# Kernel tuning notes

Hardware: AMD Instinct MI355X
Metric: run time of the kernel (lower is better)

Reference implementation:

```python
import jax, jax.numpy as jnp
import numpy as np

D_MODEL = 1024
NUM_HEADS = 16
D_K = D_MODEL // NUM_HEADS
THETA = 10000.0
BATCH = 2
SEQ = 2048


def apply_rope(x, token_positions):
    # x: [B, H, S, D_K]; token_positions: [S] int
    half = D_K // 2
    inv_freq = THETA ** (-(jnp.arange(half, dtype=jnp.float32) * 2.0) / D_K)  # [half]
    angles = token_positions.astype(jnp.float32)[:, None] * inv_freq[None, :]  # [S, half]
    cos = jnp.cos(angles)  # [S, half]
    sin = jnp.sin(angles)
    x1 = x[..., 0::2]  # even indices
    x2 = x[..., 1::2]  # odd indices
    out_even = x1 * cos - x2 * sin
    out_odd = x1 * sin + x2 * cos
    # interleave back: [..., S, half, 2] -> [..., S, D_K]
    return jnp.stack([out_even, out_odd], axis=-1).reshape(x.shape)


def setup_inputs() -> dict:
    key = jax.random.key(0)
    ks = jax.random.split(key, 5)
    x = jax.random.normal(ks[0], (BATCH, SEQ, D_MODEL), dtype=jnp.float32)
    token_positions = jnp.arange(SEQ, dtype=jnp.int64)
    scale = 0.02
    Wq = jax.random.normal(ks[1], (D_MODEL, D_MODEL), dtype=jnp.float32) * scale
    Wk = jax.random.normal(ks[2], (D_MODEL, D_MODEL), dtype=jnp.float32) * scale
    Wv = jax.random.normal(ks[3], (D_MODEL, D_MODEL), dtype=jnp.float32) * scale
    Wo = jax.random.normal(ks[4], (D_MODEL, D_MODEL), dtype=jnp.float32) * scale
    return {"x": x, "token_positions": token_positions, "Wq": Wq, "Wk": Wk, "Wv": Wv, "Wo": Wo}


def reference(x, token_positions, Wq, Wk, Wv, Wo):
    B, S, _ = x.shape
    # cs336 Linear: y = x @ W.T with W of shape (out, in), no bias
    def proj(W):
        h = jnp.einsum('bsd,od->bso', x, W)
        return h.reshape(B, S, NUM_HEADS, D_K).transpose(0, 2, 1, 3)  # [B,H,S,Dk]
    Q = apply_rope(proj(Wq), token_positions)
    K = apply_rope(proj(Wk), token_positions)
    V = proj(Wv)
    scores = jnp.einsum('bhqd,bhkd->bhqk', Q, K) / jnp.sqrt(jnp.float32(D_K))
    causal = jnp.tril(jnp.ones((S, S), dtype=bool))
    scores = jnp.where(causal, scores, -jnp.inf)
    attn = jax.nn.softmax(scores, axis=-1)
    out = jnp.einsum('bhqk,bhkd->bhqd', attn, V)  # [B,H,S,Dk]
    out = out.transpose(0, 2, 1, 3).reshape(B, S, D_MODEL)
    return jnp.einsum('bsd,od->bso', out, Wo)
```

## Files before the change

kernel.cpp:

```cpp
#include <hip/hip_runtime.h>
#include <hip/hip_bf16.h>
#include <math.h>

#define NHEADS 16
#define DKH 64
#define SEQ 2048
#define DMODEL 1024

typedef __attribute__((ext_vector_type(8))) short short8;
typedef __attribute__((ext_vector_type(4))) float f32x4;

#define GLDS16(g, l)                                         \
  __builtin_amdgcn_global_load_lds(                          \
      (__attribute__((address_space(1))) void*)(void*)(g),   \
      (__attribute__((address_space(3))) void*)(l), 16, 0, 0)

__device__ __forceinline__ short f2bf(float f) {
  unsigned u = __float_as_uint(f);
  unsigned r = (u + 0x7fffu + ((u >> 16) & 1u)) >> 16;
  return (short)r;
}

__device__ __forceinline__ short8 pack8(float4 a, float4 b) {
  short8 v;
  v[0] = f2bf(a.x); v[1] = f2bf(a.y); v[2] = f2bf(a.z); v[3] = f2bf(a.w);
  v[4] = f2bf(b.x); v[5] = f2bf(b.y); v[6] = f2bf(b.z); v[7] = f2bf(b.w);
  return v;
}

__device__ __forceinline__ int swz(int r, int gran) {
  return r * 64 + ((gran ^ (r & 7)) << 3);
}

__global__ __launch_bounds__(256) void precast_rope_kernel(
    const float* __restrict__ X, const float* __restrict__ Wq,
    const float* __restrict__ Wk, const float* __restrict__ Wv,
    const float* __restrict__ Wo, const int* __restrict__ tp,
    short* __restrict__ Xb, short* __restrict__ Wqb, short* __restrict__ Wkb,
    short* __restrict__ Wvb, short* __restrict__ Wob,
    float* __restrict__ ct, float* __restrict__ st) {
  int bid = blockIdx.x;
  if (bid < 4096) {
    int i = bid * 256 + threadIdx.x;
    const float* src; short* dst; int off;
    if (i < 524288) { src = X; dst = Xb; off = i; }
    else {
      int k = i - 524288; int w = k >> 17; off = k & 131071;
      src = (w == 0) ? Wq : (w == 1) ? Wk : (w == 2) ? Wv : Wo;
      dst = (w == 0) ? Wqb : (w == 1) ? Wkb : (w == 2) ? Wvb : Wob;
    }
    const float4* p = reinterpret_cast<const float4*>(src) + 2 * (size_t)off;
    float4 a = p[0], b = p[1];
    reinterpret_cast<short8*>(dst)[off] = pack8(a, b);
  } else {
    int idx = (bid - 4096) * 256 + threadIdx.x;
    if (idx >= SEQ * 32) return;
    int s = idx >> 5, i = idx & 31;
    int is64 = (tp[1] == 0);
    int p = is64 ? tp[2 * s] : tp[s];
    float invf = powf(10000.0f, -(2.0f * (float)i) / 64.0f);
    float a = (float)p * invf;
    ct[idx] = cosf(a);
    st[idx] = sinf(a);
  }
}

__global__ __launch_bounds__(512, 2) void gemm_qkv_kernel(
    const short* __restrict__ X, const short* __restrict__ Wq,
    const short* __restrict__ Wk, const short* __restrict__ Wv,
    short* __restrict__ Qb, short* __restrict__ Kb, short* __restrict__ Vb,
    const float* __restrict__ ct, const float* __restrict__ st) {
  __shared__ __align__(16) short As[2][256 * 64];
  __shared__ __align__(16) short Bs[2][256 * 64];
  const int tm = blockIdx.x;
  const int tn = blockIdx.y;
  const int tid = threadIdx.x;
  const int wave = tid >> 6, lane = tid & 63;
  const int l15 = lane & 15, quad = lane >> 4;
  const int wm = wave >> 2, wn = wave & 3;

  const int mid = tn >> 2;
  const int n0 = (tn & 3) * 256;
  const short* W = (mid == 0) ? Wq : (mid == 1 ? Wk : Wv);
  const short* Abase = X + (size_t)(tm * 256) * DMODEL;
  const short* Bbase = W + (size_t)n0 * DMODEL;

  const int lr = lane >> 3;
  const int lc = (lane & 7) ^ lr;

#define STG(SRC, DST, bufi, half, kt_)                                     \
  do {                                                                     \
    int R0 = (half) * 128 + wave * 16;                                     \
    GLDS16((SRC) + (size_t)(R0 + lr) * DMODEL + (kt_) * 64 + lc * 8,       \
           &DST[bufi][R0 * 64 + lane * 8]);                                \
    GLDS16((SRC) + (size_t)(R0 + 8 + lr) * DMODEL + (kt_) * 64 + lc * 8,   \
           &DST[bufi][(R0 + 8) * 64 + lane * 8]);                          \
  } while (0)

  f32x4 acc[8][4];
#pragma unroll
  for (int m = 0; m < 8; m++)
#pragma unroll
    for (int n = 0; n < 4; n++) acc[m][n] = (f32x4){0.f, 0.f, 0.f, 0.f};

  STG(Bbase, Bs, 0, 0, 0); STG(Bbase, Bs, 0, 1, 0);
  STG(Abase, As, 0, 0, 0); STG(Abase, As, 0, 1, 0);
  STG(Bbase, Bs, 1, 0, 1); STG(Bbase, Bs, 1, 1, 1);

  short8 bfr[4][2];
  for (int kt = 0; kt < 16; kt++) {
    const int buf = kt & 1;
    if (kt < 15) { STG(Abase, As, buf ^ 1, 0, kt + 1); }
    if (kt < 15) { asm volatile("s_waitcnt vmcnt(6)" ::: "memory"); }
    else         { asm volatile("s_waitcnt vmcnt(0)" ::: "memory"); }
    asm volatile("s_barrier" ::: "memory");
#pragma unroll
    for (int nb = 0; nb < 4; nb++)
#pragma unroll
      for (int ks = 0; ks < 2; ks++)
        bfr[nb][ks] = *reinterpret_cast<const short8*>(
            &Bs[buf][swz(wn * 64 + nb * 16 + l15, ks * 4 + quad)]);
    {
      short8 af[2][2];
#pragma unroll
      for (int j = 0; j < 2; j++)
#pragma unroll
        for (int ks = 0; ks < 2; ks++)
          af[j][ks] = *reinterpret_cast<const short8*>(
              &As[buf][swz(wm * 128 + j * 16 + l15, ks * 4 + quad)]);
      __builtin_amdgcn_s_setprio(1);
#pragma unroll
      for (int j = 0; j < 2; j++)
#pragma unroll
        for (int nb = 0; nb < 4; nb++)
#pragma unroll
          for (int ks = 0; ks < 2; ks++)
            acc[j][nb] = __builtin_amdgcn_mfma_f32_16x16x32_bf16(
                af[j][ks], bfr[nb][ks], acc[j][nb], 0, 0, 0);
      __builtin_amdgcn_s_setprio(0);
    }
    asm volatile("s_barrier" ::: "memory");
#pragma unroll
    for (int p = 1; p < 4; p++) {
      short8 af[2][2];
#pragma unroll
      for (int j = 0; j < 2; j++)
#pragma unroll
        for (int ks = 0; ks < 2; ks++)
          af[j][ks] = *reinterpret_cast<const short8*>(
              &As[buf][swz(wm * 128 + (p * 2 + j) * 16 + l15, ks * 4 + quad)]);
      if (p == 1)      { if (kt < 15) { STG(Abase, As, buf ^ 1, 1, kt + 1); } }
      else if (p == 2) { if (kt < 14) { STG(Bbase, Bs, buf, 0, kt + 2); } }
      else             { if (kt < 14) { STG(Bbase, Bs, buf, 1, kt + 2); } }
      asm volatile("s_barrier" ::: "memory");
      __builtin_amdgcn_s_setprio(1);
#pragma unroll
      for (int j = 0; j < 2; j++)
#pragma unroll
        for (int nb = 0; nb < 4; nb++)
#pragma unroll
          for (int ks = 0; ks < 2; ks++)
            acc[p * 2 + j][nb] = __builtin_amdgcn_mfma_f32_16x16x32_bf16(
                af[j][ks], bfr[nb][ks], acc[p * 2 + j][nb], 0, 0, 0);
      __builtin_amdgcn_s_setprio(0);
      asm volatile("s_barrier" ::: "memory");
    }
  }
#undef STG

#pragma unroll
  for (int mf = 0; mf < 8; mf++) {
    const int s0g = tm * 256 + wm * 128 + mf * 16 + quad * 4;
    const int b = s0g >> 11, s = s0g & 2047;
#pragma unroll
    for (int nb = 0; nb < 4; nb++) {
      int nl = n0 + wn * 64 + nb * 16 + l15;
      int h = nl >> 6, dd = nl & 63;
      if (mid == 2) {
        unsigned u0 = (unsigned)(unsigned short)f2bf(acc[mf][nb][0]) |
                      ((unsigned)(unsigned short)f2bf(acc[mf][nb][1]) << 16);
        unsigned u1 = (unsigned)(unsigned short)f2bf(acc[mf][nb][2]) |
                      ((unsigned)(unsigned short)f2bf(acc[mf][nb][3]) << 16);
        uint2 pk; pk.x = u0; pk.y = u1;
        *reinterpret_cast<uint2*>(Vb + ((size_t)(b * NHEADS + h) * DKH + dd) * SEQ + s) = pk;
      } else {
#pragma unroll
        for (int reg = 0; reg < 4; reg++) {
          float v = acc[mf][nb][reg];
          float pv = __shfl_xor(v, 1);
          int fi = dd >> 1;
          int sg = s + reg;
          float c = ct[sg * 32 + fi], sn = st[sg * 32 + fi];
          float o = (dd & 1) ? (pv * sn + v * c) : (v * c - pv * sn);
          size_t oi = (((size_t)(b * NHEADS + h)) * SEQ + sg) * DKH + dd;
          ((mid == 0) ? Qb : Kb)[oi] = f2bf(o);
        }
      }
    }
  }
}

__global__ __launch_bounds__(256, 4) void attn_kernel(
    const short* __restrict__ Qb, const short* __restrict__ Kb,
    const short* __restrict__ Vtb, short* __restrict__ Ob) {
  __shared__ __align__(16) short QPs[64 * 64];
  __shared__ __align__(16) short Ks[2][64 * 64];
  __shared__ __align__(16) short Vs[2][64 * 64];

  const int id = blockIdx.x;
  const int xx = id & 7;
  const int mm = (((id >> 3) & 3) + (id >> 8)) & 3;
  const int bh = id >> 5;
  const int qt = (mm == 0) ? (31 - xx) : (mm == 1) ? (16 + xx)
               : (mm == 2) ? (15 - xx) : xx;

  const int tid = threadIdx.x;
  const int wave = tid >> 6, lane = tid & 63;
  const int l15 = lane & 15, quad = lane >> 4;
  const int sr0 = tid >> 3, sc = tid & 7;

  const short* Qp = Qb + (size_t)bh * SEQ * DKH;
  const short* Kp = Kb + (size_t)bh * SEQ * DKH;
  const short* Vp = Vtb + (size_t)bh * DKH * SEQ;

  uint4 kreg[2], vreg[2];
#pragma unroll
  for (int i = 0; i < 2; i++) {
    int r = sr0 + i * 32;
    kreg[i] = *reinterpret_cast<const uint4*>(Kp + (size_t)r * DKH + sc * 8);
    vreg[i] = *reinterpret_cast<const uint4*>(Vp + (size_t)r * SEQ + sc * 8);
  }
#pragma unroll
  for (int i = 0; i < 2; i++) {
    int r = sr0 + i * 32;
    uint4 v = *reinterpret_cast<const uint4*>(Qp + (size_t)(qt * 64 + r) * DKH + sc * 8);
    *reinterpret_cast<uint4*>(&QPs[swz(r, sc)]) = v;
  }
#pragma unroll
  for (int i = 0; i < 2; i++) {
    int r = sr0 + i * 32;
    *reinterpret_cast<uint4*>(&Ks[0][swz(r, sc)]) = kreg[i];
    *reinterpret_cast<uint4*>(&Vs[0][swz(r, sc)]) = vreg[i];
  }
  __syncthreads();
  short8 qf0, qf1;
  {
    int r = wave * 16 + l15;
    qf0 = *reinterpret_cast<const short8*>(&QPs[swz(r, quad)]);
    qf1 = *reinterpret_cast<const short8*>(&QPs[swz(r, 4 + quad)]);
  }

  f32x4 accO[4];
#pragma unroll
  for (int i = 0; i < 4; i++) accO[i] = (f32x4){0.f, 0.f, 0.f, 0.f};
  float rs = 0.f;

  const float SCL = 0.125f * 1.44269504089f;
  const float FM = 13.0f;

  int buf = 0;
  for (int kt = 0; kt <= qt; kt++) {
    if (kt < qt) {
#pragma unroll
      for (int i = 0; i < 2; i++) {
        int r = sr0 + i * 32;
        kreg[i] = *reinterpret_cast<const uint4*>(Kp + (size_t)((kt + 1) * 64 + r) * DKH + sc * 8);
        vreg[i] = *reinterpret_cast<const uint4*>(Vp + (size_t)r * SEQ + (kt + 1) * 64 + sc * 8);
      }
    }

    f32x4 sa[4];
#pragma unroll
    for (int nb = 0; nb < 4; nb++) {
      sa[nb] = (f32x4){0.f, 0.f, 0.f, 0.f};
      int r = nb * 16 + l15;
      short8 kf0 = *reinterpret_cast<const short8*>(&Ks[buf][swz(r, quad)]);
      sa[nb] = __builtin_amdgcn_mfma_f32_16x16x32_bf16(kf0, qf0, sa[nb], 0, 0, 0);
      short8 kf1 = *reinterpret_cast<const short8*>(&Ks[buf][swz(r, 4 + quad)]);
      sa[nb] = __builtin_amdgcn_mfma_f32_16x16x32_bf16(kf1, qf1, sa[nb], 0, 0, 0);
    }

    const bool diag = (kt == qt);
    const int prow = wave * 16 + l15;
#pragma unroll
    for (int nb = 0; nb < 4; nb++) {
      float p0 = exp2f(sa[nb][0] * SCL - FM);
      float p1 = exp2f(sa[nb][1] * SCL - FM);
      float p2 = exp2f(sa[nb][2] * SCL - FM);
      float p3 = exp2f(sa[nb][3] * SCL - FM);
      if (diag) {
        int kbase = nb * 16 + quad * 4;
        if (kbase + 0 > prow) p0 = 0.f;
        if (kbase + 1 > prow) p1 = 0.f;
        if (kbase + 2 > prow) p2 = 0.f;
        if (kbase + 3 > prow) p3 = 0.f;
      }
      rs += (p0 + p1) + (p2 + p3);
      unsigned u0 = (unsigned)(unsigned short)f2bf(p0) |
                    ((unsigned)(unsigned short)f2bf(p1) << 16);
      unsigned u1 = (unsigned)(unsigned short)f2bf(p2) |
                    ((unsigned)(unsigned short)f2bf(p3) << 16);
      uint2 pk; pk.x = u0; pk.y = u1;
      int g = 2 * nb + (quad >> 1);
      *reinterpret_cast<uint2*>(&QPs[swz(prow, g) + (quad & 1) * 4]) = pk;
    }

    short8 pf0 = *reinterpret_cast<const short8*>(&QPs[swz(prow, quad)]);
    short8 pf1 = *reinterpret_cast<const short8*>(&QPs[swz(prow, 4 + quad)]);
#pragma unroll
    for (int db = 0; db < 4; db++) {
      int dv = db * 16 + l15;
      short8 vf0 = *reinterpret_cast<const short8*>(&Vs[buf][swz(dv, quad)]);
      accO[db] = __builtin_amdgcn_mfma_f32_16x16x32_bf16(pf0, vf0, accO[db], 0, 0, 0);
      short8 vf1 = *reinterpret_cast<const short8*>(&Vs[buf][swz(dv, 4 + quad)]);
      accO[db] = __builtin_amdgcn_mfma_f32_16x16x32_bf16(pf1, vf1, accO[db], 0, 0, 0);
    }

    if (kt < qt) {
      int nbuf = buf ^ 1;
#pragma unroll
      for (int i = 0; i < 2; i++) {
        int r = sr0 + i * 32;
        *reinterpret_cast<uint4*>(&Ks[nbuf][swz(r, sc)]) = kreg[i];
        *reinterpret_cast<uint4*>(&Vs[nbuf][swz(r, sc)]) = vreg[i];
      }
      __syncthreads();
      buf = nbuf;
    }
  }

  float t = rs;
  t += __shfl_xor(t, 16);
  t += __shfl_xor(t, 32);
  float lv[4];
#pragma unroll
  for (int reg = 0; reg < 4; reg++) lv[reg] = __shfl(t, quad * 4 + reg);

  int b = bh >> 4, h = bh & 15;
#pragma unroll
  for (int db = 0; db < 4; db++)
#pragma unroll
    for (int reg = 0; reg < 4; reg++) {
      int s = qt * 64 + wave * 16 + quad * 4 + reg;
      int dv = db * 16 + l15;
      float o = accO[db][reg] / lv[reg];
      Ob[((size_t)(b * SEQ + s)) * DMODEL + h * DKH + dv] = f2bf(o);
    }
}

__global__ __launch_bounds__(256) void gemm_out_kernel(
    const short* __restrict__ X, const short* __restrict__ Wo, float* __restrict__ Out) {
  __shared__ __align__(16) short As[128 * 64];
  __shared__ __align__(16) short Bs[64 * 64];
  const int tm = blockIdx.x;
  const int tn = blockIdx.y;
  const int tid = threadIdx.x;
  const int wave = tid >> 6, lane = tid & 63;
  const int l15 = lane & 15, quad = lane >> 4;
  const int wm = wave >> 1, wn = wave & 1;

  const short* Abase = X + (size_t)(tm * 128) * DMODEL;
  const short* Bbase = Wo + (size_t)(tn * 64) * DMODEL;

  const int lr = lane >> 3;
  const int lc = (lane & 7) ^ lr;

  f32x4 acc[4][2];
#pragma unroll
  for (int mb = 0; mb < 4; mb++)
#pragma unroll
    for (int nb = 0; nb < 2; nb++) acc[mb][nb] = (f32x4){0.f, 0.f, 0.f, 0.f};

  for (int kk = 0; kk < 16; kk++) {
    const short* Ak = Abase + kk * 64;
    const short* Bk = Bbase + kk * 64;
#pragma unroll
    for (int i = 0; i < 4; i++) {
      int R = i * 32 + wave * 8;
      GLDS16(Ak + (size_t)(R + lr) * DMODEL + lc * 8, &As[R * 64 + lane * 8]);
    }
#pragma unroll
    for (int i = 0; i < 2; i++) {
      int R = i * 32 + wave * 8;
      GLDS16(Bk + (size_t)(R + lr) * DMODEL + lc * 8, &Bs[R * 64 + lane * 8]);
    }
    __syncthreads();
#pragma unroll
    for (int kg = 0; kg < 2; kg++) {
      short8 af[4], bf[2];
#pragma unroll
      for (int mb = 0; mb < 4; mb++) {
        int r = wm * 64 + mb * 16 + l15;
        af[mb] = *reinterpret_cast<const short8*>(&As[swz(r, kg * 4 + quad)]);
      }
#pragma unroll
      for (int nb = 0; nb < 2; nb++) {
        int r = wn * 32 + nb * 16 + l15;
        bf[nb] = *reinterpret_cast<const short8*>(&Bs[swz(r, kg * 4 + quad)]);
      }
#pragma unroll
      for (int mb = 0; mb < 4; mb++)
#pragma unroll
        for (int nb = 0; nb < 2; nb++)
          acc[mb][nb] = __builtin_amdgcn_mfma_f32_16x16x32_bf16(af[mb], bf[nb], acc[mb][nb], 0, 0, 0);
    }
    __syncthreads();
  }
#pragma unroll
  for (int mb = 0; mb < 4; mb++)
#pragma unroll
    for (int nb = 0; nb < 2; nb++)
#pragma unroll
      for (int reg = 0; reg < 4; reg++) {
        int rg = tm * 128 + wm * 64 + mb * 16 + quad * 4 + reg;
        int col = tn * 64 + wn * 32 + nb * 16 + l15;
        Out[(size_t)rg * DMODEL + col] = acc[mb][nb][reg];
      }
}

extern "C" void kernel_launch(void* const* d_in, const int* in_sizes, int n_in,
                              void* d_out, int out_size, void* d_ws, size_t ws_size,
                              hipStream_t stream) {
  (void)in_sizes; (void)n_in; (void)out_size; (void)ws_size;
  const float* X  = (const float*)d_in[0];
  const int*   tp = (const int*)d_in[1];
  const float* Wq = (const float*)d_in[2];
  const float* Wk = (const float*)d_in[3];
  const float* Wv = (const float*)d_in[4];
  const float* Wo = (const float*)d_in[5];
  float* Out = (float*)d_out;

  short* Qb  = (short*)d_ws;
  short* Kb  = Qb + 4194304;
  short* Vb  = Kb + 4194304;
  short* Ab  = Vb + 4194304;
  short* Xb  = Ab + 4194304;
  short* Wqb = Xb + 4194304;
  short* Wkb = Wqb + 1048576;
  short* Wvb = Wkb + 1048576;
  short* Wob = Wvb + 1048576;
  float* ct  = (float*)(Wob + 1048576);
  float* st  = ct + SEQ * 32;

  precast_rope_kernel<<<dim3(4352), dim3(256), 0, stream>>>(
      X, Wq, Wk, Wv, Wo, tp, Xb, Wqb, Wkb, Wvb, Wob, ct, st);
  gemm_qkv_kernel<<<dim3(16, 12), dim3(512), 0, stream>>>(Xb, Wqb, Wkb, Wvb,
                                                          Qb, Kb, Vb, ct, st);
  attn_kernel<<<dim3(1024), dim3(256), 0, stream>>>(Qb, Kb, Vb, Ab);
  gemm_out_kernel<<<dim3(32, 16), dim3(256), 0, stream>>>(Ab, Wob, Out);
}
```

Baseline: 195.9 us.

## Retile QKV GEMM to 256x192 tiles filling all CUs with XCD-aware mapping

```diff
diff --git a/kernel.cpp b/kernel.cpp
--- a/kernel.cpp
+++ b/kernel.cpp
@@ -71,55 +71,62 @@
     short* __restrict__ Qb, short* __restrict__ Kb, short* __restrict__ Vb,
     const float* __restrict__ ct, const float* __restrict__ st) {
   __shared__ __align__(16) short As[2][256 * 64];
-  __shared__ __align__(16) short Bs[2][256 * 64];
-  const int tm = blockIdx.x;
-  const int tn = blockIdx.y;
+  __shared__ __align__(16) short Bs[2][192 * 64];
+  const int id = blockIdx.x;
+  const int xcd = id & 7, rr = id >> 3;
+  const int tm = (xcd & 3) * 4 + (rr & 3);
+  const int tn = (xcd >> 2) * 8 + (rr >> 2);
   const int tid = threadIdx.x;
   const int wave = tid >> 6, lane = tid & 63;
   const int l15 = lane & 15, quad = lane >> 4;
   const int wm = wave >> 2, wn = wave & 3;
 
-  const int mid = tn >> 2;
-  const int n0 = (tn & 3) * 256;
-  const short* W = (mid == 0) ? Wq : (mid == 1 ? Wk : Wv);
+  const int n0 = tn * 192;
   const short* Abase = X + (size_t)(tm * 256) * DMODEL;
-  const short* Bbase = W + (size_t)n0 * DMODEL;
+  const short* Bbase = Wq + (size_t)n0 * DMODEL;
+  (void)Wk; (void)Wv;
 
   const int lr = lane >> 3;
   const int lc = (lane & 7) ^ lr;
 
-#define STG(SRC, DST, bufi, half, kt_)                                     \
+#define STGA(bufi, half, kt_)                                              \
   do {                                                                     \
     int R0 = (half) * 128 + wave * 16;                                     \
-    GLDS16((SRC) + (size_t)(R0 + lr) * DMODEL + (kt_) * 64 + lc * 8,       \
-           &DST[bufi][R0 * 64 + lane * 8]);                                \
-    GLDS16((SRC) + (size_t)(R0 + 8 + lr) * DMODEL + (kt_) * 64 + lc * 8,   \
-           &DST[bufi][(R0 + 8) * 64 + lane * 8]);                          \
+    GLDS16(Abase + (size_t)(R0 + lr) * DMODEL + (kt_) * 64 + lc * 8,       \
+           &As[bufi][R0 * 64 + lane * 8]);                                 \
+    GLDS16(Abase + (size_t)(R0 + 8 + lr) * DMODEL + (kt_) * 64 + lc * 8,   \
+           &As[bufi][(R0 + 8) * 64 + lane * 8]);                           \
   } while (0)
-
-  f32x4 acc[8][4];
+#define STGB(bufi, t, kt_)                                                 \
+  do {                                                                     \
+    int R0 = (t) * 64 + wave * 8;                                          \
+    GLDS16(Bbase + (size_t)(R0 + lr) * DMODEL + (kt_) * 64 + lc * 8,       \
+           &Bs[bufi][R0 * 64 + lane * 8]);                                 \
+  } while (0)
+
+  f32x4 acc[8][3];
 #pragma unroll
   for (int m = 0; m < 8; m++)
 #pragma unroll
-    for (int n = 0; n < 4; n++) acc[m][n] = (f32x4){0.f, 0.f, 0.f, 0.f};
-
-  STG(Bbase, Bs, 0, 0, 0); STG(Bbase, Bs, 0, 1, 0);
-  STG(Abase, As, 0, 0, 0); STG(Abase, As, 0, 1, 0);
-  STG(Bbase, Bs, 1, 0, 1); STG(Bbase, Bs, 1, 1, 1);
-
-  short8 bfr[4][2];
+    for (int n = 0; n < 3; n++) acc[m][n] = (f32x4){0.f, 0.f, 0.f, 0.f};
+
+  STGB(0, 0, 0); STGB(0, 1, 0); STGB(0, 2, 0);
+  STGA(0, 0, 0); STGA(0, 1, 0);
+  STGB(1, 0, 1); STGB(1, 1, 1); STGB(1, 2, 1);
+
+  short8 bfr[3][2];
   for (int kt = 0; kt < 16; kt++) {
     const int buf = kt & 1;
-    if (kt < 15) { STG(Abase, As, buf ^ 1, 0, kt + 1); }
-    if (kt < 15) { asm volatile("s_waitcnt vmcnt(6)" ::: "memory"); }
+    if (kt < 15) { STGA(buf ^ 1, 0, kt + 1); }
+    if (kt < 15) { asm volatile("s_waitcnt vmcnt(5)" ::: "memory"); }
     else         { asm volatile("s_waitcnt vmcnt(0)" ::: "memory"); }
     asm volatile("s_barrier" ::: "memory");
 #pragma unroll
-    for (int nb = 0; nb < 4; nb++)
+    for (int nb = 0; nb < 3; nb++)
 #pragma unroll
       for (int ks = 0; ks < 2; ks++)
         bfr[nb][ks] = *reinterpret_cast<const short8*>(
-            &Bs[buf][swz(wn * 64 + nb * 16 + l15, ks * 4 + quad)]);
+            &Bs[buf][swz(wn * 48 + nb * 16 + l15, ks * 4 + quad)]);
     {
       short8 af[2][2];
 #pragma unroll
@@ -132,7 +139,7 @@
 #pragma unroll
       for (int j = 0; j < 2; j++)
 #pragma unroll
-        for (int nb = 0; nb < 4; nb++)
+        for (int nb = 0; nb < 3; nb++)
 #pragma unroll
           for (int ks = 0; ks < 2; ks++)
             acc[j][nb] = __builtin_amdgcn_mfma_f32_16x16x32_bf16(
@@ -149,15 +156,15 @@
         for (int ks = 0; ks < 2; ks++)
           af[j][ks] = *reinterpret_cast<const short8*>(
               &As[buf][swz(wm * 128 + (p * 2 + j) * 16 + l15, ks * 4 + quad)]);
-      if (p == 1)      { if (kt < 15) { STG(Abase, As, buf ^ 1, 1, kt + 1); } }
-      else if (p == 2) { if (kt < 14) { STG(Bbase, Bs, buf, 0, kt + 2); } }
-      else             { if (kt < 14) { STG(Bbase, Bs, buf, 1, kt + 2); } }
+      if (p == 1)      { if (kt < 15) { STGA(buf ^ 1, 1, kt + 1); } }
+      else if (p == 2) { if (kt < 14) { STGB(buf, 0, kt + 2); STGB(buf, 1, kt + 2); } }
+      else             { if (kt < 14) { STGB(buf, 2, kt + 2); } }
       asm volatile("s_barrier" ::: "memory");
       __builtin_amdgcn_s_setprio(1);
 #pragma unroll
       for (int j = 0; j < 2; j++)
 #pragma unroll
-        for (int nb = 0; nb < 4; nb++)
+        for (int nb = 0; nb < 3; nb++)
 #pragma unroll
           for (int ks = 0; ks < 2; ks++)
             acc[p * 2 + j][nb] = __builtin_amdgcn_mfma_f32_16x16x32_bf16(
@@ -166,16 +173,19 @@
       asm volatile("s_barrier" ::: "memory");
     }
   }
-#undef STG
+#undef STGA
+#undef STGB
 
 #pragma unroll
   for (int mf = 0; mf < 8; mf++) {
     const int s0g = tm * 256 + wm * 128 + mf * 16 + quad * 4;
     const int b = s0g >> 11, s = s0g & 2047;
 #pragma unroll
-    for (int nb = 0; nb < 4; nb++) {
-      int nl = n0 + wn * 64 + nb * 16 + l15;
-      int h = nl >> 6, dd = nl & 63;
+    for (int nb = 0; nb < 3; nb++) {
+      int nl = n0 + wn * 48 + nb * 16 + l15;
+      int mid = nl >> 10;
+      int c = nl & 1023;
+      int h = c >> 6, dd = c & 63;
       if (mid == 2) {
         unsigned u0 = (unsigned)(unsigned short)f2bf(acc[mf][nb][0]) |
                       ((unsigned)(unsigned short)f2bf(acc[mf][nb][1]) << 16);
@@ -190,8 +200,8 @@
           float pv = __shfl_xor(v, 1);
           int fi = dd >> 1;
           int sg = s + reg;
-          float c = ct[sg * 32 + fi], sn = st[sg * 32 + fi];
-          float o = (dd & 1) ? (pv * sn + v * c) : (v * c - pv * sn);
+          float cc = ct[sg * 32 + fi], sn = st[sg * 32 + fi];
+          float o = (dd & 1) ? (pv * sn + v * cc) : (v * cc - pv * sn);
           size_t oi = (((size_t)(b * NHEADS + h)) * SEQ + sg) * DKH + dd;
           ((mid == 0) ? Qb : Kb)[oi] = f2bf(o);
         }
@@ -444,8 +454,8 @@
 
   precast_rope_kernel<<<dim3(4352), dim3(256), 0, stream>>>(
       X, Wq, Wk, Wv, Wo, tp, Xb, Wqb, Wkb, Wvb, Wob, ct, st);
-  gemm_qkv_kernel<<<dim3(16, 12), dim3(512), 0, stream>>>(Xb, Wqb, Wkb, Wvb,
-                                                          Qb, Kb, Vb, ct, st);
+  gemm_qkv_kernel<<<dim3(256), dim3(512), 0, stream>>>(Xb, Wqb, Wkb, Wvb,
+                                                       Qb, Kb, Vb, ct, st);
   attn_kernel<<<dim3(1024), dim3(256), 0, stream>>>(Qb, Kb, Vb, Ab);
   gemm_out_kernel<<<dim3(32, 16), dim3(256), 0, stream>>>(Ab, Wob, Out);
 }
```

New measurement: 183.1 us. 1.07x faster.
